# Optimization experiments

Hardware: AMD Instinct MI355X
Metric: run time of the kernel (lower is better)

Reference implementation:

```python
import jax, jax.numpy as jnp
import numpy as np

N, E = 50000, 800000
IN, HID, H, OUT = 128, 32, 8, 64
HD = HID * H  # 256
EPS = 1e-5


def _p(key, shape, scale=0.05):
    return jax.random.normal(key, shape, dtype=jnp.float32) * scale


def setup_inputs() -> dict:
    key = jax.random.key(0)
    ks = jax.random.split(key, 32)
    inp = {
        'x': jax.random.normal(ks[0], (N, IN), dtype=jnp.float32),
        'edge_index': jax.random.randint(ks[1], (2, E), 0, N, dtype=jnp.int64),
        'edge_attr': jax.random.normal(ks[2], (E, 1), dtype=jnp.float32),
        # layer 1 (TransformerConv: in=128 -> heads*hid=256)
        'Wq1': _p(ks[3], (IN, HD)), 'bq1': jnp.zeros((HD,), jnp.float32),
        'Wk1': _p(ks[4], (IN, HD)), 'bk1': jnp.zeros((HD,), jnp.float32),
        'Wv1': _p(ks[5], (IN, HD)), 'bv1': jnp.zeros((HD,), jnp.float32),
        'We1': _p(ks[6], (1, HD)),  # lin_edge, no bias in PyG
        'Ws1': _p(ks[7], (IN, HD)), 'bs1': jnp.zeros((HD,), jnp.float32),  # root/skip
        'lnw1': jnp.ones((HD,), jnp.float32), 'lnb1': jnp.zeros((HD,), jnp.float32),
        # layer 2 (in=256 -> 256)
        'Wq2': _p(ks[8], (HD, HD)), 'bq2': jnp.zeros((HD,), jnp.float32),
        'Wk2': _p(ks[9], (HD, HD)), 'bk2': jnp.zeros((HD,), jnp.float32),
        'Wv2': _p(ks[10], (HD, HD)), 'bv2': jnp.zeros((HD,), jnp.float32),
        'We2': _p(ks[11], (1, HD)),
        'Ws2': _p(ks[12], (HD, HD)), 'bs2': jnp.zeros((HD,), jnp.float32),
        'lnw2': jnp.ones((HD,), jnp.float32), 'lnb2': jnp.zeros((HD,), jnp.float32),
        # output linear 256 -> 64
        'Wo': _p(ks[13], (HD, OUT)), 'bo': jnp.zeros((OUT,), jnp.float32),
    }
    return inp


def transformer_conv(x, src, dst, edge_attr, Wq, bq, Wk, bk, Wv, bv, We, Ws, bs):
    n = x.shape[0]
    q = (x @ Wq + bq).reshape(n, H, HID)
    k = (x @ Wk + bk).reshape(n, H, HID)
    v = (x @ Wv + bv).reshape(n, H, HID)
    e = (edge_attr @ We).reshape(-1, H, HID)            # [E,H,d]
    kj = k[src] + e                                     # gather + edge key
    score = jnp.einsum('ehd,ehd->eh', q[dst], kj) / np.sqrt(HID)  # [E,H]
    # segment softmax over destination nodes
    m = jax.ops.segment_max(score, dst, num_segments=n)  # [N,H]
    ex = jnp.exp(score - m[dst])
    s = jax.ops.segment_sum(ex, dst, num_segments=n)
    alpha = ex / s[dst]                                  # [E,H]
    msg = alpha[..., None] * (v[src] + e)                # [E,H,d]
    out = jax.ops.segment_sum(msg, dst, num_segments=n).reshape(n, HD)
    return out + x @ Ws + bs                             # root weight skip


def graph_layernorm(x, w, b):
    # PyG LayerNorm, mode='graph': global mean/std over all nodes & features
    xc = x - x.mean()
    out = xc / (xc.std() + EPS)
    return out * w + b


def reference(x, edge_index, edge_attr,
              Wq1, bq1, Wk1, bk1, Wv1, bv1, We1, Ws1, bs1, lnw1, lnb1,
              Wq2, bq2, Wk2, bk2, Wv2, bv2, We2, Ws2, bs2, lnw2, lnb2,
              Wo, bo):
    src, dst = edge_index[0], edge_index[1]
    h = transformer_conv(x, src, dst, edge_attr, Wq1, bq1, Wk1, bk1, Wv1, bv1, We1, Ws1, bs1)
    h = jax.nn.elu(graph_layernorm(h, lnw1, lnb1))
    h = transformer_conv(h, src, dst, edge_attr, Wq2, bq2, Wk2, bk2, Wv2, bv2, We2, Ws2, bs2)
    h = jax.nn.elu(graph_layernorm(h, lnw2, lnb2))
    return h @ Wo + bo
```

## Files before the change

### kernel.cpp

```cpp
#include <hip/hip_runtime.h>
#include <hip/hip_fp16.h>
#include <math.h>

#define IN_DIM 128
#define HD 256
#define EPSLN 1e-5f

typedef _Float16 half8 __attribute__((ext_vector_type(8)));
typedef float f32x4 __attribute__((ext_vector_type(4)));
typedef float f32x2 __attribute__((ext_vector_type(2)));

__device__ inline void store4(float* p, float4 o) { *(float4*)p = o; }
__device__ inline void store4(__half* p, float4 o) {
    union { uint2 u; __half2 h[2]; } s;
    s.h[0] = __floats2half2_rn(o.x, o.y);
    s.h[1] = __floats2half2_rn(o.z, o.w);
    *(uint2*)p = s.u;
}
__device__ inline float4 h4_to_f4(uint2 u) {
    union { unsigned int w; __half2 h; } a, b;
    a.w = u.x; b.w = u.y;
    float2 lo = __half22float2(a.h), hi = __half22float2(b.h);
    return make_float4(lo.x, lo.y, hi.x, hi.y);
}
__device__ inline unsigned int f4_to_fp8x4(float a, float b, float c, float d) {
    int v = 0;
    v = __builtin_amdgcn_cvt_pk_fp8_f32(a, b, v, false);
    v = __builtin_amdgcn_cvt_pk_fp8_f32(c, d, v, true);
    return (unsigned int)v;
}
__device__ inline float4 fp8x4_to_f4(unsigned int u) {
    f32x2 lo = __builtin_amdgcn_cvt_pk_f32_fp8((int)u, false);
    f32x2 hi = __builtin_amdgcn_cvt_pk_f32_fp8((int)u, true);
    return make_float4(lo.x, lo.y, hi.x, hi.y);
}

__device__ inline void async_copy16(const __half* g, _Float16* l) {
    __builtin_amdgcn_global_load_lds(
        (const __attribute__((address_space(1))) void*)g,
        (__attribute__((address_space(3))) void*)l,
        16, 0, 0);
}

__device__ inline void unpermute_col(int n, int& sel, int& c) {
    if (n < 256) { sel = 0; c = n; }
    else if (n < 768) {
        int j = n - 256, chunk = j >> 3, w = j & 7;
        if (w < 4) { sel = 1; c = chunk * 4 + w; }
        else       { sel = 2; c = chunk * 4 + w - 4; }
    } else { sel = 3; c = n - 768; }
}

__global__ void prep_k(
    const float4* __restrict__ x, __half* __restrict__ xh, int total4,
    const int* __restrict__ dst, int* __restrict__ counts, int* __restrict__ rank, int E,
    const float* __restrict__ Wq1, const float* __restrict__ Wk1,
    const float* __restrict__ Wv1, const float* __restrict__ Ws1,
    const float* __restrict__ Wq2, const float* __restrict__ Wk2,
    const float* __restrict__ Wv2, const float* __restrict__ Ws2,
    const float* __restrict__ Wo,
    const float* __restrict__ bq1, const float* __restrict__ bk1,
    const float* __restrict__ bv1, const float* __restrict__ bs1,
    const float* __restrict__ bq2, const float* __restrict__ bk2,
    const float* __restrict__ bv2, const float* __restrict__ bs2,
    __half* __restrict__ Wc1, __half* __restrict__ Wc2, __half* __restrict__ Wot,
    float* __restrict__ bc1, float* __restrict__ bc2)
{
    int idx = blockIdx.x * 256 + threadIdx.x;
    if (idx < total4) store4(xh + (size_t)idx * 4, x[idx]);
    if (idx < E) rank[idx] = atomicAdd(&counts[dst[idx]], 1);
    if (idx < 131072) {
        int n = idx >> 7, k = idx & 127;
        int sel, c; unpermute_col(n, sel, c);
        const float* W = (sel == 0) ? Wq1 : (sel == 1) ? Wk1 : (sel == 2) ? Wv1 : Ws1;
        Wc1[idx] = __float2half(W[(size_t)k * 256 + c]);
    } else if (idx < 393216) {
        int j = idx - 131072;
        int n = j >> 8, k = j & 255;
        int sel, c; unpermute_col(n, sel, c);
        const float* W = (sel == 0) ? Wq2 : (sel == 1) ? Wk2 : (sel == 2) ? Wv2 : Ws2;
        Wc2[j] = __float2half(W[(size_t)k * 256 + c]);
    } else if (idx < 409600) {
        int j = idx - 393216;
        int n = j >> 8, k = j & 255;
        Wot[j] = __float2half(Wo[(size_t)k * 64 + n]);
    } else if (idx < 410624) {
        int n = idx - 409600;
        int sel, c; unpermute_col(n, sel, c);
        const float* b = (sel == 0) ? bq1 : (sel == 1) ? bk1 : (sel == 2) ? bv1 : bs1;
        bc1[n] = b[c];
    } else if (idx < 411648) {
        int n = idx - 410624;
        int sel, c; unpermute_col(n, sel, c);
        const float* b = (sel == 0) ? bq2 : (sel == 1) ? bk2 : (sel == 2) ? bv2 : bs2;
        bc2[n] = b[c];
    }
}

#define BM 128
#define BN 128
#define TROWB 272

__global__ __launch_bounds__(256) void gemm_mfma(
    const __half* __restrict__ A, const __half* __restrict__ Wt,
    const float* __restrict__ bias, __half* __restrict__ C,
    unsigned char* __restrict__ kv8,
    int M, int K, int Nc)
{
    __shared__ char smem[BM * TROWB];

    int tid = threadIdx.x;
    int lane = tid & 63, w = tid >> 6;
    int wm = w >> 1, wn = w & 1;
    int quad = lane >> 4, l16 = lane & 15;
    int nbx = (int)gridDim.x >> 3;
    int wkr = ((int)blockIdx.x & 7) * nbx + ((int)blockIdx.x >> 3);
    int row0 = (wkr >> 3) * BM;
    int col0 = (wkr & 7) * BN;

    f32x4 acc[4][4];
#pragma unroll
    for (int i = 0; i < 4; i++)
#pragma unroll
        for (int j = 0; j < 4; j++) acc[i][j] = (f32x4){0.f, 0.f, 0.f, 0.f};

    int srow = lane >> 2;
    int schunk = lane & 3;

    int nt = K >> 5;

    auto STAGE = [&](int step, int buf) {
        int k0 = step << 5;
        _Float16* Asb = (_Float16*)(smem + buf * 16384);
        _Float16* Bsb = (_Float16*)(smem + 8192 + buf * 16384);
#pragma unroll
        for (int t = 0; t < 2; t++) {
            int r = w * 32 + t * 16 + srow;
            int gr = row0 + r; if (gr > M - 1) gr = M - 1;
            int gchunk = schunk ^ ((r ^ (r >> 2)) & 3);
            async_copy16(&A[(size_t)gr * K + k0 + gchunk * 8], &Asb[(w * 32 + t * 16) * 32]);
        }
#pragma unroll
        for (int t = 0; t < 2; t++) {
            int r = w * 32 + t * 16 + srow;
            int gc = col0 + r; if (gc > Nc - 1) gc = Nc - 1;
            int gchunk = schunk ^ ((r ^ (r >> 2)) & 3);
            async_copy16(&Wt[(size_t)gc * K + k0 + gchunk * 8], &Bsb[(w * 32 + t * 16) * 32]);
        }
    };

    STAGE(0, 0);
    __syncthreads();

    for (int t = 0; t < nt; ++t) {
        if (t + 1 < nt) STAGE(t + 1, (t + 1) & 1);
        _Float16* Asb = (_Float16*)(smem + (t & 1) * 16384);
        _Float16* Bsb = (_Float16*)(smem + 8192 + (t & 1) * 16384);
        half8 af[4], bf[4];
#pragma unroll
        for (int i = 0; i < 4; i++) {
            int ra = wm * 64 + i * 16 + l16;
            af[i] = *(half8*)&Asb[ra * 32 + ((quad ^ ((ra ^ (ra >> 2)) & 3)) * 8)];
            int rb = wn * 64 + i * 16 + l16;
            bf[i] = *(half8*)&Bsb[rb * 32 + ((quad ^ ((rb ^ (rb >> 2)) & 3)) * 8)];
        }
#pragma unroll
        for (int i = 0; i < 4; i++)
#pragma unroll
            for (int j = 0; j < 4; j++)
                acc[i][j] = __builtin_amdgcn_mfma_f32_16x16x32_f16(af[i], bf[j], acc[i][j], 0, 0, 0);
        __syncthreads();
    }

#pragma unroll
    for (int j = 0; j < 4; j++) {
        int tcol = wn * 64 + j * 16 + l16;
        float bb = (col0 + tcol < Nc) ? bias[col0 + tcol] : 0.f;
#pragma unroll
        for (int i = 0; i < 4; i++) {
#pragma unroll
            for (int r = 0; r < 4; r++) {
                int trow = wm * 64 + i * 16 + quad * 4 + r;
                ((__half*)(smem + trow * TROWB))[tcol] = __float2half(acc[i][j][r] + bb);
            }
        }
    }
    __syncthreads();
    bool iskv = (col0 >= 256) && (col0 < 768);
    int crow = tid >> 4, cchunk = tid & 15;
    for (int p = 0; p < 8; p++) {
        int trow = p * 16 + crow;
        int grow = row0 + trow;
        if (grow >= M) continue;
        uint4 val = *(uint4*)(smem + trow * TROWB + cchunk * 16);
        if (iskv) {
            float4 lo = h4_to_f4(make_uint2(val.x, val.y));
            float4 hi = h4_to_f4(make_uint2(val.z, val.w));
            uint2 o8;
            o8.x = f4_to_fp8x4(lo.x, lo.y, lo.z, lo.w);
            o8.y = f4_to_fp8x4(hi.x, hi.y, hi.z, hi.w);
            *(uint2*)&kv8[(size_t)grow * 512 + (col0 - 256) + cchunk * 8] = o8;
        } else {
            *(uint4*)&C[(size_t)grow * Nc + col0 + cchunk * 8] = val;
        }
    }
}

__global__ __launch_bounds__(256) void gemm_out_k(
    const __half* __restrict__ A, const __half* __restrict__ Wot,
    const float* __restrict__ bias, float* __restrict__ D, int M)
{
    __shared__ _Float16 smem[12288];
    int tid = threadIdx.x;
    int lane = tid & 63, w = tid >> 6;
    int quad = lane >> 4, l16 = lane & 15;
    int row0 = blockIdx.x * 128;
    const int K = 256;

    f32x4 acc[2][4];
#pragma unroll
    for (int i = 0; i < 2; i++)
#pragma unroll
        for (int j = 0; j < 4; j++) acc[i][j] = (f32x4){0.f, 0.f, 0.f, 0.f};

    int srow = lane >> 2;
    int schunk = lane & 3;
    const int nt = 8;

    auto STAGE = [&](int step, int buf) {
        int k0 = step << 5;
        _Float16* Asb = smem + buf * 4096;
        _Float16* Bsb = smem + 8192 + buf * 2048;
#pragma unroll
        for (int t = 0; t < 2; t++) {
            int r = w * 32 + t * 16 + srow;
            int gr = row0 + r; if (gr > M - 1) gr = M - 1;
            int gchunk = schunk ^ ((r ^ (r >> 2)) & 3);
            async_copy16(&A[(size_t)gr * K + k0 + gchunk * 8], &Asb[(w * 32 + t * 16) * 32]);
        }
        {
            int r = w * 16 + srow;
            int gchunk = schunk ^ ((r ^ (r >> 2)) & 3);
            async_copy16(&Wot[(size_t)r * K + k0 + gchunk * 8], &Bsb[(w * 16) * 32]);
        }
    };

    STAGE(0, 0);
    __syncthreads();

    for (int t = 0; t < nt; ++t) {
        if (t + 1 < nt) STAGE(t + 1, (t + 1) & 1);
        _Float16* Asb = smem + (t & 1) * 4096;
        _Float16* Bsb = smem + 8192 + (t & 1) * 2048;
        half8 af[2], bf[4];
#pragma unroll
        for (int i = 0; i < 2; i++) {
            int ra = w * 32 + i * 16 + l16;
            af[i] = *(half8*)&Asb[ra * 32 + ((quad ^ ((ra ^ (ra >> 2)) & 3)) * 8)];
        }
#pragma unroll
        for (int j = 0; j < 4; j++) {
            int rb = j * 16 + l16;
            bf[j] = *(half8*)&Bsb[rb * 32 + ((quad ^ ((rb ^ (rb >> 2)) & 3)) * 8)];
        }
#pragma unroll
        for (int i = 0; i < 2; i++)
#pragma unroll
            for (int j = 0; j < 4; j++)
                acc[i][j] = __builtin_amdgcn_mfma_f32_16x16x32_f16(af[i], bf[j], acc[i][j], 0, 0, 0);
        __syncthreads();
    }

#pragma unroll
    for (int i = 0; i < 2; i++) {
#pragma unroll
        for (int j = 0; j < 4; j++) {
            int gcol = j * 16 + l16;
            float bb = bias[gcol];
#pragma unroll
            for (int r = 0; r < 4; r++) {
                int grow = row0 + w * 32 + i * 16 + quad * 4 + r;
                if (grow < M) D[(size_t)grow * 64 + gcol] = acc[i][j][r] + bb;
            }
        }
    }
}

__global__ __launch_bounds__(1024) void scan_k(const int* __restrict__ counts,
                                               int* __restrict__ offs, int n)
{
    __shared__ int wsum[16];
    __shared__ int wpre[16];
    int tid = threadIdx.x, lane = tid & 63, wid = tid >> 6;
    int per = (n + 1023) / 1024;
    int start = tid * per, end = min(start + per, n);
    int sum = 0;
    for (int i = start; i < end; i++) sum += counts[i];
    int v = sum;
#pragma unroll
    for (int d = 1; d < 64; d <<= 1) {
        int t = __shfl_up(v, (unsigned)d, 64);
        if (lane >= d) v += t;
    }
    if (lane == 63) wsum[wid] = v;
    __syncthreads();
    if (tid == 0) {
        int acc = 0;
        for (int i = 0; i < 16; i++) { wpre[i] = acc; acc += wsum[i]; }
    }
    __syncthreads();
    int pre = wpre[wid] + v - sum;
    for (int i = start; i < end; i++) { offs[i] = pre; pre += counts[i]; }
    if (end == n && start <= n) offs[n] = pre;
}

__global__ void scatter_k(const int* __restrict__ src, const int* __restrict__ dst,
                          const float* __restrict__ attr, const int* __restrict__ offs,
                          const int* __restrict__ rank, int2* __restrict__ edat, int E)
{
    int e = blockIdx.x * 256 + threadIdx.x;
    if (e < 8) edat[E + e] = make_int2(0, 0);
    if (e < E) {
        int p = offs[dst[e]] + rank[e];
        edat[p] = make_int2(src[e], __float_as_int(attr[e]));
    }
}

__global__ __launch_bounds__(256) void attn_k(
    const uint2* __restrict__ q2, const uint2* __restrict__ kv8u2,
    const float* __restrict__ We,
    __half* __restrict__ hwork, const int2* __restrict__ edat,
    const int* __restrict__ offs,
    double* __restrict__ stats, int n, int nGroups)
{
    int lane = threadIdx.x & 63;
    int wid = threadIdx.x >> 6;
    float4 we = ((const float4*)We)[lane];
    float tsum = 0.f, tsq = 0.f;

    for (int g = blockIdx.x; g < nGroups; g += gridDim.x) {
        int node = g * 4 + wid;
        if (node >= n) continue;
        float4 qv = h4_to_f4(q2[(size_t)node * 256 + lane]);
        float qwe = qv.x * we.x + qv.y * we.y + qv.z * we.z + qv.w * we.w;
        qwe += __shfl_xor(qwe, 1);
        qwe += __shfl_xor(qwe, 2);
        qwe += __shfl_xor(qwe, 4);

        float4 accv = make_float4(0.f, 0.f, 0.f, 0.f);
        float sat = 0.f;
        float m = -INFINITY, l = 0.f;
        int i0 = __builtin_amdgcn_readfirstlane(offs[node]);
        int i1 = __builtin_amdgcn_readfirstlane(offs[node + 1]);

        int abA[8], srA[8], abB[8], srB[8];
        uint2 kvA[8], kvB[8];

        auto LOADB = [&](int base, int* ab_, int* sr_, uint2* kv_) {
#pragma unroll
            for (int u = 0; u < 8; u++) {
                int2 ed = edat[base + u];
                sr_[u] = __builtin_amdgcn_readfirstlane(ed.x);
                ab_[u] = __builtin_amdgcn_readfirstlane(ed.y);
            }
#pragma unroll
            for (int u = 0; u < 8; u++)
                kv_[u] = (kv8u2 + (size_t)(unsigned)sr_[u] * 64)[lane];
        };

        auto COMPUTE = [&](const int* ab_, const uint2* kv_, int cnt) {
            float pv[8];
#pragma unroll
            for (int u = 0; u < 8; u++) {
                float4 kvf = fp8x4_to_f4(kv_[u].x);
                float p = qv.x * kvf.x + qv.y * kvf.y + qv.z * kvf.z + qv.w * kvf.w;
                p += __shfl_xor(p, 1);
                p += __shfl_xor(p, 2);
                p += __shfl_xor(p, 4);
                p = fmaf(__int_as_float(ab_[u]), qwe, p) * 0.17677669529663687f;
                pv[u] = (u < cnt) ? p : -INFINITY;
            }
            float m01 = fmaxf(pv[0], pv[1]), m23 = fmaxf(pv[2], pv[3]);
            float m45 = fmaxf(pv[4], pv[5]), m67 = fmaxf(pv[6], pv[7]);
            float pmax = fmaxf(fmaxf(m01, m23), fmaxf(m45, m67));
            float mn = fmaxf(m, pmax);
            float corr = __expf(m - mn);
            l *= corr;
            sat *= corr;
            accv.x *= corr; accv.y *= corr; accv.z *= corr; accv.w *= corr;
#pragma unroll
            for (int u = 0; u < 8; u++) {
                float wgt = __expf(pv[u] - mn);
                l += wgt;
                sat = fmaf(wgt, __int_as_float(ab_[u]), sat);
                float4 vv = fp8x4_to_f4(kv_[u].y);
                accv.x = fmaf(wgt, vv.x, accv.x);
                accv.y = fmaf(wgt, vv.y, accv.y);
                accv.z = fmaf(wgt, vv.z, accv.z);
                accv.w = fmaf(wgt, vv.w, accv.w);
            }
            m = mn;
        };

        if (i0 < i1) {
            int i = i0;
            LOADB(i, abA, srA, kvA);
            while (true) {
                if (i + 8 >= i1) { COMPUTE(abA, kvA, i1 - i); break; }
                LOADB(i + 8, abB, srB, kvB);
                COMPUTE(abA, kvA, 8);
                i += 8;
                if (i + 8 >= i1) { COMPUTE(abB, kvB, i1 - i); break; }
                LOADB(i + 8, abA, srA, kvA);
                COMPUTE(abB, kvB, 8);
                i += 8;
            }
        }

        float inv = (l > 0.f) ? 1.f / l : 0.f;
        float4 sk = h4_to_f4(q2[(size_t)node * 256 + 192 + lane]);
        float sw = sat * inv;
        float4 o;
        o.x = fmaf(accv.x, inv, fmaf(sw, we.x, sk.x));
        o.y = fmaf(accv.y, inv, fmaf(sw, we.y, sk.y));
        o.z = fmaf(accv.z, inv, fmaf(sw, we.z, sk.z));
        o.w = fmaf(accv.w, inv, fmaf(sw, we.w, sk.w));
        store4(hwork + (size_t)node * 256 + lane * 4, o);
        tsum += o.x + o.y + o.z + o.w;
        tsq += o.x * o.x + o.y * o.y + o.z * o.z + o.w * o.w;
    }

#pragma unroll
    for (int d = 1; d < 64; d <<= 1) {
        tsum += __shfl_xor(tsum, d);
        tsq += __shfl_xor(tsq, d);
    }
    __shared__ float red[8];
    if (lane == 0) { red[wid] = tsum; red[4 + wid] = tsq; }
    __syncthreads();
    if (threadIdx.x == 0) {
        double s = (double)red[0] + (double)red[1] + (double)red[2] + (double)red[3];
        double sq = (double)red[4] + (double)red[5] + (double)red[6] + (double)red[7];
        atomicAdd(&stats[0], s);
        atomicAdd(&stats[1], sq);
    }
}

__global__ __launch_bounds__(256) void ln_apply(
    const uint2* __restrict__ in, __half* __restrict__ out,
    const float4* __restrict__ w4, const float4* __restrict__ b4,
    const double* __restrict__ stats, double cnt, int total4)
{
    int base = (blockIdx.x * 256 + threadIdx.x) * 4;
    if (base >= total4) return;
    double mu = stats[0] / cnt;
    double var = stats[1] / cnt - mu * mu;
    if (var < 0.0) var = 0.0;
    float mean = (float)mu;
    float inv = (float)(1.0 / (sqrt(var) + (double)EPSLN));
#pragma unroll
    for (int u = 0; u < 4; u++) {
        int i = base + u;
        if (i >= total4) return;
        int c = i & 63;
        float4 xv = h4_to_f4(in[i]);
        float4 w = w4[c], b = b4[c];
        float4 o;
        o.x = fmaf((xv.x - mean) * inv, w.x, b.x);
        o.y = fmaf((xv.y - mean) * inv, w.y, b.y);
        o.z = fmaf((xv.z - mean) * inv, w.z, b.z);
        o.w = fmaf((xv.w - mean) * inv, w.w, b.w);
        o.x = o.x > 0.f ? o.x : expm1f(o.x);
        o.y = o.y > 0.f ? o.y : expm1f(o.y);
        o.z = o.z > 0.f ? o.z : expm1f(o.z);
        o.w = o.w > 0.f ? o.w : expm1f(o.w);
        store4(out + (size_t)i * 4, o);
    }
}

extern "C" void kernel_launch(void* const* d_in, const int* in_sizes, int n_in,
                              void* d_out, int out_size, void* d_ws, size_t ws_size,
                              hipStream_t stream)
{
    const float* x      = (const float*)d_in[0];
    const int*   ei     = (const int*)d_in[1];
    const float* eattr  = (const float*)d_in[2];
    const float* Wq1 = (const float*)d_in[3];  const float* bq1 = (const float*)d_in[4];
    const float* Wk1 = (const float*)d_in[5];  const float* bk1 = (const float*)d_in[6];
    const float* Wv1 = (const float*)d_in[7];  const float* bv1 = (const float*)d_in[8];
    const float* We1 = (const float*)d_in[9];
    const float* Ws1 = (const float*)d_in[10]; const float* bs1 = (const float*)d_in[11];
    const float* lnw1 = (const float*)d_in[12]; const float* lnb1 = (const float*)d_in[13];
    const float* Wq2 = (const float*)d_in[14]; const float* bq2 = (const float*)d_in[15];
    const float* Wk2 = (const float*)d_in[16]; const float* bk2 = (const float*)d_in[17];
    const float* Wv2 = (const float*)d_in[18]; const float* bv2 = (const float*)d_in[19];
    const float* We2 = (const float*)d_in[20];
    const float* Ws2 = (const float*)d_in[21]; const float* bs2 = (const float*)d_in[22];
    const float* lnw2 = (const float*)d_in[23]; const float* lnb2 = (const float*)d_in[24];
    const float* Wo  = (const float*)d_in[25]; const float* bo  = (const float*)d_in[26];

    const int N = in_sizes[0] / IN_DIM;
    const int E = in_sizes[2];
    const int* esrc = ei;
    const int* edst = ei + E;

    char* ws = (char*)d_ws;
    size_t off = 0;
    auto alloc = [&](size_t bytes) -> char* {
        char* p = ws + off;
        off += (bytes + 255) / 256 * 256;
        return p;
    };
    int*    counts = (int*)alloc((size_t)N * 4);
    double* stats  = (double*)alloc(64);
    size_t zbytes = off;
    int*    rank   = (int*)alloc((size_t)E * 4);
    int*    offs   = (int*)alloc((size_t)(N + 1) * 4);
    int2*   edat   = (int2*)alloc((size_t)(E + 8) * 8);
    __half* xh     = (__half*)alloc((size_t)N * IN_DIM * 2);
    __half* qkvs   = (__half*)alloc((size_t)N * 1024 * 2);
    unsigned char* kv8 = (unsigned char*)alloc((size_t)N * 512);
    __half* hwork  = (__half*)alloc((size_t)N * HD * 2);
    __half* hio    = (__half*)alloc((size_t)N * HD * 2);
    __half* Wc1    = (__half*)alloc((size_t)1024 * IN_DIM * 2);
    __half* Wc2    = (__half*)alloc((size_t)1024 * HD * 2);
    __half* Wot    = (__half*)alloc((size_t)64 * HD * 2);
    float*  bc1    = (float*)alloc(1024 * 4);
    float*  bc2    = (float*)alloc(1024 * 4);

    hipMemsetAsync(d_ws, 0, zbytes, stream);

    int total4x = N * (IN_DIM / 4);
    int prepWork = total4x > E ? total4x : E;
    if (prepWork < 411648) prepWork = 411648;
    prep_k<<<(prepWork + 255) / 256, 256, 0, stream>>>(
        (const float4*)x, xh, total4x, edst, counts, rank, E,
        Wq1, Wk1, Wv1, Ws1, Wq2, Wk2, Wv2, Ws2, Wo,
        bq1, bk1, bv1, bs1, bq2, bk2, bv2, bs2,
        Wc1, Wc2, Wot, bc1, bc2);

    scan_k<<<1, 1024, 0, stream>>>(counts, offs, N);
    scatter_k<<<(E + 255) / 256, 256, 0, stream>>>(esrc, edst, eattr, offs, rank,
                                                   edat, E);

    int nbx = (N + BM - 1) / BM;
    dim3 gqkvs(nbx * 8);
    int nGroups = (N + 3) / 4;
    int gaBlocks = nGroups < 2048 ? nGroups : 2048;
    int total4 = N * (HD / 4);
    dim3 gl((total4 / 4 + 255) / 256);
    dim3 gout((N + 127) / 128);

    gemm_mfma<<<gqkvs, 256, 0, stream>>>(xh, Wc1, bc1, qkvs, kv8, N, IN_DIM, 1024);
    attn_k<<<gaBlocks, 256, 0, stream>>>((const uint2*)qkvs, (const uint2*)kv8, We1,
                                         hwork, edat, offs, stats, N, nGroups);
    ln_apply<<<gl, 256, 0, stream>>>((const uint2*)hwork, hio,
                                     (const float4*)lnw1, (const float4*)lnb1,
                                     stats, (double)N * HD, total4);

    gemm_mfma<<<gqkvs, 256, 0, stream>>>(hio, Wc2, bc2, qkvs, kv8, N, HD, 1024);
    attn_k<<<gaBlocks, 256, 0, stream>>>((const uint2*)qkvs, (const uint2*)kv8, We2,
                                         hwork, edat, offs, stats + 2, N, nGroups);
    ln_apply<<<gl, 256, 0, stream>>>((const uint2*)hwork, hio,
                                     (const float4*)lnw2, (const float4*)lnb2,
                                     stats + 2, (double)N * HD, total4);

    gemm_out_k<<<gout, 256, 0, stream>>>(hio, Wot, bo, (float*)d_out, N);
}
```

Measured before the change: 573.9 us.

## Replace single-block scan with three-pass multi-block scan; vectorize ln_apply I/O

The single 1024-thread block prefix scan over node counts, in which each thread walked about 49 counts serially, is replaced by a three-kernel reduce/scan-top/fix-up scan spread over about 98 blocks. ln_apply now computes the mean and inverse std once per block into shared memory and uses 16-byte vector loads and stores instead of 8-byte ones. The scan change removes a serial bottleneck at the cost of two extra launches. The ln_apply change drops the per-element bounds check, so it assumes total4 is a multiple of 4.

```diff
diff --git a/kernel.cpp b/kernel.cpp
--- a/kernel.cpp
+++ b/kernel.cpp
@@ -286,32 +286,67 @@
     }
 }
 
-__global__ __launch_bounds__(1024) void scan_k(const int* __restrict__ counts,
-                                               int* __restrict__ offs, int n)
-{
-    __shared__ int wsum[16];
-    __shared__ int wpre[16];
-    int tid = threadIdx.x, lane = tid & 63, wid = tid >> 6;
-    int per = (n + 1023) / 1024;
-    int start = tid * per, end = min(start + per, n);
-    int sum = 0;
-    for (int i = start; i < end; i++) sum += counts[i];
-    int v = sum;
+__global__ __launch_bounds__(256) void scan_part_k(const int* __restrict__ counts,
+                                                   int* __restrict__ part, int n)
+{
+    int b = blockIdx.x, t = threadIdx.x;
+    int i0 = b * 512 + t * 2;
+    int s = 0;
+    if (i0 < n) s += counts[i0];
+    if (i0 + 1 < n) s += counts[i0 + 1];
+    int lane = t & 63, wid = t >> 6;
+    int v = s;
+#pragma unroll
+    for (int d = 1; d < 64; d <<= 1) v += __shfl_xor(v, d);
+    __shared__ int ws[4];
+    if (lane == 0) ws[wid] = v;
+    __syncthreads();
+    if (t == 0) part[b] = ws[0] + ws[1] + ws[2] + ws[3];
+}
+
+__global__ __launch_bounds__(128) void scan_top_k(int* __restrict__ part, int nb)
+{
+    int t = threadIdx.x, lane = t & 63, wid = t >> 6;
+    int orig = (t < nb) ? part[t] : 0;
+    int v = orig;
 #pragma unroll
     for (int d = 1; d < 64; d <<= 1) {
-        int t = __shfl_up(v, (unsigned)d, 64);
-        if (lane >= d) v += t;
-    }
+        int u = __shfl_up(v, (unsigned)d, 64);
+        if (lane >= d) v += u;
+    }
+    __shared__ int wsum[2];
     if (lane == 63) wsum[wid] = v;
     __syncthreads();
-    if (tid == 0) {
-        int acc = 0;
-        for (int i = 0; i < 16; i++) { wpre[i] = acc; acc += wsum[i]; }
-    }
-    __syncthreads();
-    int pre = wpre[wid] + v - sum;
-    for (int i = start; i < end; i++) { offs[i] = pre; pre += counts[i]; }
-    if (end == n && start <= n) offs[n] = pre;
+    int add = (wid == 1) ? wsum[0] : 0;
+    if (t < nb) part[t] = v + add - orig;
+}
+
+__global__ __launch_bounds__(256) void scan_fix_k(const int* __restrict__ counts,
+                                                  const int* __restrict__ part,
+                                                  int* __restrict__ offs, int n)
+{
+    int b = blockIdx.x, t = threadIdx.x;
+    int lane = t & 63, wid = t >> 6;
+    int i0 = b * 512 + t * 2;
+    int c0 = (i0 < n) ? counts[i0] : 0;
+    int c1 = (i0 + 1 < n) ? counts[i0 + 1] : 0;
+    int s = c0 + c1;
+    int v = s;
+#pragma unroll
+    for (int d = 1; d < 64; d <<= 1) {
+        int u = __shfl_up(v, (unsigned)d, 64);
+        if (lane >= d) v += u;
+    }
+    __shared__ int wsum[4], wpre[4];
+    if (lane == 63) wsum[wid] = v;
+    __syncthreads();
+    if (t == 0) { int a = 0; for (int i = 0; i < 4; i++) { wpre[i] = a; a += wsum[i]; } }
+    __syncthreads();
+    int pre = part[b] + wpre[wid] + v - s;
+    if (i0 < n) offs[i0] = pre;
+    if (i0 + 1 < n) offs[i0 + 1] = pre + c0;
+    int end = i0 + 2; if (end > n) end = n;
+    if (end == n) offs[n] = pre + c0 + c1;
 }
 
 __global__ void scatter_k(const int* __restrict__ src, const int* __restrict__ dst,
@@ -451,19 +486,30 @@
     const float4* __restrict__ w4, const float4* __restrict__ b4,
     const double* __restrict__ stats, double cnt, int total4)
 {
+    __shared__ float sm[2];
+    if (threadIdx.x == 0) {
+        double mu = stats[0] / cnt;
+        double var = stats[1] / cnt - mu * mu;
+        if (var < 0.0) var = 0.0;
+        sm[0] = (float)mu;
+        sm[1] = (float)(1.0 / (sqrt(var) + (double)EPSLN));
+    }
+    __syncthreads();
     int base = (blockIdx.x * 256 + threadIdx.x) * 4;
     if (base >= total4) return;
-    double mu = stats[0] / cnt;
-    double var = stats[1] / cnt - mu * mu;
-    if (var < 0.0) var = 0.0;
-    float mean = (float)mu;
-    float inv = (float)(1.0 / (sqrt(var) + (double)EPSLN));
+    float mean = sm[0];
+    float inv = sm[1];
+
+    uint4 ra = *(const uint4*)(in + base);
+    uint4 rb = *(const uint4*)(in + base + 2);
+    uint2 rw[4] = { make_uint2(ra.x, ra.y), make_uint2(ra.z, ra.w),
+                    make_uint2(rb.x, rb.y), make_uint2(rb.z, rb.w) };
+    uint2 ow[4];
 #pragma unroll
     for (int u = 0; u < 4; u++) {
         int i = base + u;
-        if (i >= total4) return;
         int c = i & 63;
-        float4 xv = h4_to_f4(in[i]);
+        float4 xv = h4_to_f4(rw[u]);
         float4 w = w4[c], b = b4[c];
         float4 o;
         o.x = fmaf((xv.x - mean) * inv, w.x, b.x);
@@ -474,8 +520,15 @@
         o.y = o.y > 0.f ? o.y : expm1f(o.y);
         o.z = o.z > 0.f ? o.z : expm1f(o.z);
         o.w = o.w > 0.f ? o.w : expm1f(o.w);
-        store4(out + (size_t)i * 4, o);
-    }
+        union { uint2 u2; __half2 h[2]; } s;
+        s.h[0] = __floats2half2_rn(o.x, o.y);
+        s.h[1] = __floats2half2_rn(o.z, o.w);
+        ow[u] = s.u2;
+    }
+    uint4 s0 = make_uint4(ow[0].x, ow[0].y, ow[1].x, ow[1].y);
+    uint4 s1 = make_uint4(ow[2].x, ow[2].y, ow[3].x, ow[3].y);
+    *(uint4*)(out + (size_t)base * 4) = s0;
+    *(uint4*)(out + (size_t)(base + 2) * 4) = s1;
 }
 
 extern "C" void kernel_launch(void* const* d_in, const int* in_sizes, int n_in,
@@ -527,6 +580,7 @@
     __half* Wot    = (__half*)alloc((size_t)64 * HD * 2);
     float*  bc1    = (float*)alloc(1024 * 4);
     float*  bc2    = (float*)alloc(1024 * 4);
+    int*    part   = (int*)alloc(512);
 
     hipMemsetAsync(d_ws, 0, zbytes, stream);
 
@@ -539,7 +593,10 @@
         bq1, bk1, bv1, bs1, bq2, bk2, bv2, bs2,
         Wc1, Wc2, Wot, bc1, bc2);
 
-    scan_k<<<1, 1024, 0, stream>>>(counts, offs, N);
+    int nblkS = (N + 511) / 512;
+    scan_part_k<<<nblkS, 256, 0, stream>>>(counts, part, N);
+    scan_top_k<<<1, 128, 0, stream>>>(part, nblkS);
+    scan_fix_k<<<nblkS, 256, 0, stream>>>(counts, part, offs, N);
     scatter_k<<<(E + 255) / 256, 256, 0, stream>>>(esrc, edst, eattr, offs, rank,
                                                    edat, E);
 
```

New measurement: 497.5 us (median of 3 runs). 1.15x faster.
